# Performance work log

Measured on AMD Instinct MI355X. Metric: run time of the kernel, lower is better.

The kernel has to match this reference:

```python
import jax, jax.numpy as jnp
import numpy as np
import math

B, S, E, H = 2, 2048, 64, 8
N_LAYER = 12
EPS = 1e-5


def setup_inputs() -> dict:
    key = jax.random.key(0)
    ks = jax.random.split(key, 7)
    x = jax.random.normal(ks[0], (B, S, E), dtype=jnp.float32)
    ln_w = jnp.ones((E,), dtype=jnp.float32)
    W_q = 0.02 * jax.random.normal(ks[1], (H, E, E), dtype=jnp.float32)
    W_k = 0.02 * jax.random.normal(ks[2], (H, E, E), dtype=jnp.float32)
    W_v = 0.02 * jax.random.normal(ks[3], (H, E, E), dtype=jnp.float32)
    W_o = (0.02 / math.sqrt(2 * N_LAYER)) * jax.random.normal(ks[4], (E, H * E), dtype=jnp.float32)
    gamma = 1.0 + 0.02 * jax.random.normal(ks[5], (H, 1, 1), dtype=jnp.float32)
    return {"x": x, "ln_w": ln_w, "W_q": W_q, "W_k": W_k, "W_v": W_v, "W_o": W_o, "gamma": gamma}


def reference(x, ln_w, W_q, W_k, W_v, W_o, gamma):
    # LayerNorm (bias=False)
    mu = jnp.mean(x, axis=-1, keepdims=True)
    var = jnp.mean((x - mu) ** 2, axis=-1, keepdims=True)
    xn = (x - mu) * jax.lax.rsqrt(var + EPS) * ln_w  # [B,S,E]

    # per-head full-rank projections: x repeated across heads
    Q = jnp.einsum('bse,hef->bhsf', xn, W_q)  # [B,H,S,E]
    K = jnp.einsum('bse,hef->bhsf', xn, W_k)
    V = jnp.einsum('bse,hef->bhsf', xn, W_v)

    # RBF attention scores: exp(-gamma * ||q_i - k_j||^2 / sqrt(E)), causal
    q2 = jnp.sum(Q * Q, axis=-1)[..., :, None]          # [B,H,S,1]
    k2 = jnp.sum(K * K, axis=-1)[..., None, :]          # [B,H,1,S]
    qk = jnp.einsum('bhse,bhte->bhst', Q, K)            # [B,H,S,S]
    sqdist = q2 + k2 - 2.0 * qk
    scores = jnp.exp(-gamma[None] * sqdist / math.sqrt(E))  # gamma broadcast [H,1,1]
    causal = jnp.tril(jnp.ones((S, S), dtype=scores.dtype))
    scores = scores * causal

    out = jnp.einsum('bhst,bhte->bhse', scores, V)       # [B,H,S,E]
    out = out.transpose(0, 2, 1, 3).reshape(B, S, H * E)  # concat heads
    out = out @ W_o.T                                     # [B,S,E]
    return out
```

## Files before the change

kernel.cpp:

```cpp
#include <hip/hip_runtime.h>
#include <math.h>

typedef __attribute__((ext_vector_type(8))) short bf8;
typedef __attribute__((ext_vector_type(4))) short s4v;
typedef __attribute__((ext_vector_type(16))) float f16v;
typedef __attribute__((ext_vector_type(4))) float f4v;
typedef __attribute__((ext_vector_type(4))) int i4v;

constexpr int CS = 2048;
constexpr float EPS = 1e-5f;
constexpr float LOG2E = 1.44269504088896f;

static __device__ inline short f2bf(float x) {
  union { float f; unsigned u; } v; v.f = x;
  unsigned r = (v.u + 0x7FFFu + ((v.u >> 16) & 1u)) >> 16;
  return (short)r;
}
static __device__ inline float bf2f(short u) {
  union { unsigned u; float f; } v;
  v.u = ((unsigned)(unsigned short)u) << 16;
  return v.f;
}
static __device__ inline unsigned cvt_pk_bf16(float lo, float hi) {
  unsigned d;
  asm("v_cvt_pk_bf16_f32 %0, %1, %2" : "=v"(d) : "v"(lo), "v"(hi));
  return d;
}

__global__ __launch_bounds__(256) void k_prep(const float* __restrict__ Wq, const float* __restrict__ Wk,
                                              const float* __restrict__ Wv, const float* __restrict__ Wo,
                                              short* __restrict__ WtQ, short* __restrict__ WtK,
                                              short* __restrict__ WtV, short* __restrict__ Wob) {
  int blk = blockIdx.x, t = threadIdx.x;
  if (blk < 24) {
    __shared__ float tile[64][65];
    int w = blk >> 3, h = blk & 7;
    const float* src = (w == 0 ? Wq : w == 1 ? Wk : Wv) + h * 4096;
    short* dst = (w == 0 ? WtQ : w == 1 ? WtK : WtV) + h * 4096;
#pragma unroll
    for (int m = 0; m < 4; ++m) {
      int fi = m * 256 + t;
      int row = fi >> 4, c4 = (fi & 15) * 4;
      f4v v = *(const f4v*)&src[row * 64 + c4];
      tile[row][c4] = v.x; tile[row][c4 + 1] = v.y; tile[row][c4 + 2] = v.z; tile[row][c4 + 3] = v.w;
    }
    __syncthreads();
#pragma unroll
    for (int m = 0; m < 16; ++m) {
      int o = m * 256 + t;
      int f = o >> 6, e = o & 63;
      dst[f * 64 + e] = f2bf(tile[e][f]);
    }
  } else {
    int base = (blk - 24) * 4096;
#pragma unroll
    for (int m = 0; m < 16; ++m) {
      int o = base + m * 256 + t;
      Wob[o] = f2bf(Wo[o]);
    }
  }
}

__global__ __launch_bounds__(256) void k_qkv(const float* __restrict__ x, const float* __restrict__ ln_w,
                                             const short* __restrict__ WtQ, const short* __restrict__ WtK,
                                             const short* __restrict__ WtV, const float* __restrict__ gamma,
                                             short* __restrict__ Qf, short* __restrict__ Kf,
                                             short* __restrict__ Vf, float* __restrict__ aqg) {
  __shared__ short QtL[2 * 32 * 72];
  __shared__ short KtL[2 * 32 * 72];
  __shared__ float q2s[64];
  __shared__ float bks[64];
  int blk = blockIdx.x;
  int bh = blk & 15, st = blk >> 4;
  int b = bh >> 3, h = bh & 7;
  int t = threadIdx.x, wid = t >> 6, lane = t & 63;
  int l31 = lane & 31, g = lane >> 5;
  int sh = wid >> 1, fh = wid & 1;
  int f = fh * 32 + l31;

  int row = b * CS + st * 64 + sh * 32 + l31;
  f4v xv[8];
#pragma unroll
  for (int ks = 0; ks < 4; ++ks) {
    xv[2 * ks]     = *(const f4v*)&x[row * 64 + ks * 16 + g * 8];
    xv[2 * ks + 1] = *(const f4v*)&x[row * 64 + ks * 16 + g * 8 + 4];
  }
  float s = 0.f;
#pragma unroll
  for (int m = 0; m < 8; ++m) s += xv[m].x + xv[m].y + xv[m].z + xv[m].w;
  s += __shfl_xor(s, 32, 64);
  float mu = s * (1.f / 64.f);
  float vs = 0.f;
#pragma unroll
  for (int m = 0; m < 8; ++m) {
#pragma unroll
    for (int j = 0; j < 4; ++j) { float d = xv[m][j] - mu; vs += d * d; }
  }
  vs += __shfl_xor(vs, 32, 64);
  float rs = rsqrtf(vs * (1.f / 64.f) + EPS);
  bf8 af[4];
#pragma unroll
  for (int ks = 0; ks < 4; ++ks) {
    f4v lw0 = *(const f4v*)&ln_w[ks * 16 + g * 8];
    f4v lw1 = *(const f4v*)&ln_w[ks * 16 + g * 8 + 4];
#pragma unroll
    for (int j = 0; j < 4; ++j) {
      af[ks][j]     = f2bf((xv[2 * ks][j] - mu) * rs * lw0[j]);
      af[ks][j + 4] = f2bf((xv[2 * ks + 1][j] - mu) * rs * lw1[j]);
    }
  }
  float gh = gamma[h];
  float cgk = -gh * 0.125f * LOG2E;

  f16v cq; for (int i = 0; i < 16; ++i) cq[i] = 0.f;
#pragma unroll
  for (int ks = 0; ks < 4; ++ks) {
    bf8 bw = *(const bf8*)&WtQ[h * 4096 + f * 64 + ks * 16 + g * 8];
    cq = __builtin_amdgcn_mfma_f32_32x32x16_bf16(af[ks], bw, cq, 0, 0, 0);
  }
#pragma unroll
  for (int r = 0; r < 16; ++r) {
    int rl = (r & 3) + 8 * (r >> 2) + 4 * g;
    QtL[(sh * 32 + rl) * 72 + f] = f2bf(cq[r]);
  }
  f16v ck; for (int i = 0; i < 16; ++i) ck[i] = 0.f;
#pragma unroll
  for (int ks = 0; ks < 4; ++ks) {
    bf8 bw = *(const bf8*)&WtK[h * 4096 + f * 64 + ks * 16 + g * 8];
    ck = __builtin_amdgcn_mfma_f32_32x32x16_bf16(af[ks], bw, ck, 0, 0, 0);
  }
#pragma unroll
  for (int r = 0; r < 16; ++r) {
    int rl = (r & 3) + 8 * (r >> 2) + 4 * g;
    KtL[(sh * 32 + rl) * 72 + f] = f2bf(ck[r]);
  }
  f16v cv; for (int i = 0; i < 16; ++i) cv[i] = 0.f;
#pragma unroll
  for (int ks = 0; ks < 4; ++ks) {
    bf8 bw = *(const bf8*)&WtV[h * 4096 + f * 64 + ks * 16 + g * 8];
    cv = __builtin_amdgcn_mfma_f32_32x32x16_bf16(af[ks], bw, cv, 0, 0, 0);
  }
  __syncthreads();

  {
    int rw = t >> 2, q4 = t & 3;
    float sq = 0.f, sk = 0.f;
#pragma unroll
    for (int m = 0; m < 2; ++m) {
      bf8 vq = *(bf8*)&QtL[rw * 72 + q4 * 16 + m * 8];
      bf8 vk = *(bf8*)&KtL[rw * 72 + q4 * 16 + m * 8];
#pragma unroll
      for (int j = 0; j < 8; ++j) {
        float xq = bf2f(vq[j]); sq += xq * xq;
        float xk = bf2f(vk[j]); sk += xk * xk;
      }
    }
    sq += __shfl_xor(sq, 1, 64); sq += __shfl_xor(sq, 2, 64);
    sk += __shfl_xor(sk, 1, 64); sk += __shfl_xor(sk, 2, 64);
    if (q4 == 0) {
      q2s[rw] = sq;
      bks[rw] = exp2f(cgk * sk);
    }
  }
  {
    int ktloc = t >> 7, lm = (t >> 1) & 63, jh = t & 1;
#pragma unroll
    for (int ks = 0; ks < 4; ++ks) {
      int laddr = (ktloc * 32 + (lm & 31)) * 72 + ks * 16 + (lm >> 5) * 8 + jh * 4;
      int gaddr = ((bh * 64 + st * 2 + ktloc) * 4 + ks) * 512 + lm * 8 + jh * 4;
      *(s4v*)&Qf[gaddr] = *(s4v*)&QtL[laddr];
      *(s4v*)&Kf[gaddr] = *(s4v*)&KtL[laddr];
    }
  }
  __syncthreads();

  int kt = st * 2 + sh;
#pragma unroll
  for (int m = 0; m < 4; ++m) {
    s4v pk;
#pragma unroll
    for (int c = 0; c < 4; ++c) {
      int rl = sh * 32 + c + 8 * m + 4 * g;
      pk[c] = f2bf(cv[m * 4 + c] * bks[rl]);
    }
    int addr = ((((bh * 64 + kt) * 2 + fh) * 2 + (m >> 1)) * 64 + (m & 1) * 32 + l31) * 8 + 4 * g;
    *(s4v*)&Vf[addr] = pk;
  }
  if (t < 64) {
    aqg[bh * CS + st * 64 + t] = exp2f(cgk * q2s[t]);
  }
}

__global__ __launch_bounds__(512, 4) void k_attn(const short* __restrict__ Qf, const short* __restrict__ Kf,
                                                 const short* __restrict__ Vf, const float* __restrict__ aqg,
                                                 const float* __restrict__ gamma, short* __restrict__ attnB) {
  __shared__ float red4[4][64][37];
  int bid = blockIdx.x;
  int bh = ((bid & 7) << 1) | ((bid >> 3) & 1);
  int qt = 63 - (bid >> 4);
  int b = bh >> 3, h = bh & 7;
  int t = threadIdx.x, w = t >> 6, lane = t & 63;
  int lam = lane & 31, g = lane >> 5;
  float cg = gamma[h] * 0.25f * LOG2E;
  int L = qt + 1;
  int lo = (w * L) >> 3, hi = ((w + 1) * L) >> 3;

  bf8 qf[4];
#pragma unroll
  for (int ks = 0; ks < 4; ++ks) qf[ks] = *(const bf8*)&Qf[((bh * 64 + qt) * 4 + ks) * 512 + lane * 8];

  f16v oa0, oa1;
#pragma unroll
  for (int rr = 0; rr < 16; ++rr) { oa0[rr] = 0.f; oa1[rr] = 0.f; }

  const short* kfb = Kf + bh * 131072 + lane * 8;
  const short* vfb = Vf + bh * 131072 + lane * 8;

  for (int kt = lo; kt < hi; ++kt) {
    const short* kp = kfb + kt * 2048;
    bf8 ak0 = *(const bf8*)(kp);
    bf8 ak1 = *(const bf8*)(kp + 512);
    bf8 ak2 = *(const bf8*)(kp + 1024);
    bf8 ak3 = *(const bf8*)(kp + 1536);

    f16v ct;
#pragma unroll
    for (int rr = 0; rr < 16; ++rr) ct[rr] = 0.f;
    __builtin_amdgcn_s_setprio(1);
    ct = __builtin_amdgcn_mfma_f32_32x32x16_bf16(ak0, qf[0], ct, 0, 0, 0);
    ct = __builtin_amdgcn_mfma_f32_32x32x16_bf16(ak1, qf[1], ct, 0, 0, 0);
    ct = __builtin_amdgcn_mfma_f32_32x32x16_bf16(ak2, qf[2], ct, 0, 0, 0);
    ct = __builtin_amdgcn_mfma_f32_32x32x16_bf16(ak3, qf[3], ct, 0, 0, 0);
    __builtin_amdgcn_s_setprio(0);

    const short* vp = vfb + kt * 2048;
    bf8 av00 = *(const bf8*)(vp);
    bf8 av01 = *(const bf8*)(vp + 512);
    bf8 av10 = *(const bf8*)(vp + 1024);
    bf8 av11 = *(const bf8*)(vp + 1536);

    bool diag = (kt == qt);
    unsigned pkA[4], pkB[4];
#pragma unroll
    for (int m = 0; m < 4; ++m) {
      float sv[4];
#pragma unroll
      for (int ii = 0; ii < 4; ++ii) {
        int kloc = ii + 8 * m + 4 * g;
        float ev = exp2f(cg * ct[4 * m + ii]);
        if (diag && kloc > lam) ev = 0.f;
        sv[ii] = ev;
      }
      pkA[m] = cvt_pk_bf16(sv[0], sv[1]);
      pkB[m] = cvt_pk_bf16(sv[2], sv[3]);
    }
    __builtin_amdgcn_s_setprio(1);
#pragma unroll
    for (int ks2 = 0; ks2 < 2; ++ks2) {
      unsigned sendA = g ? pkA[2 * ks2] : pkA[2 * ks2 + 1];
      unsigned recvA = (unsigned)__shfl_xor((int)sendA, 32, 64);
      unsigned sendB = g ? pkB[2 * ks2] : pkB[2 * ks2 + 1];
      unsigned recvB = (unsigned)__shfl_xor((int)sendB, 32, 64);
      i4v wv;
      wv.x = g ? (int)recvA : (int)pkA[2 * ks2];
      wv.y = g ? (int)recvB : (int)pkB[2 * ks2];
      wv.z = g ? (int)pkA[2 * ks2 + 1] : (int)recvA;
      wv.w = g ? (int)pkB[2 * ks2 + 1] : (int)recvB;
      bf8 bs = *(bf8*)&wv;
      oa0 = __builtin_amdgcn_mfma_f32_32x32x16_bf16(ks2 ? av01 : av00, bs, oa0, 0, 0, 0);
      oa1 = __builtin_amdgcn_mfma_f32_32x32x16_bf16(ks2 ? av11 : av10, bs, oa1, 0, 0, 0);
    }
    __builtin_amdgcn_s_setprio(0);
  }

  if (w < 4) {
#pragma unroll
    for (int rr = 0; rr < 16; ++rr) {
      int e = (rr & 3) + 8 * (rr >> 2) + 4 * g;
      red4[w][e][lam] = oa0[rr];
      red4[w][e + 32][lam] = oa1[rr];
    }
  }
  __syncthreads();
  if (w >= 4) {
#pragma unroll
    for (int rr = 0; rr < 16; ++rr) {
      int e = (rr & 3) + 8 * (rr >> 2) + 4 * g;
      red4[w - 4][e][lam] += oa0[rr];
      red4[w - 4][e + 32][lam] += oa1[rr];
    }
  }
  __syncthreads();
  {
    int q = t >> 4, e0 = (t & 15) * 4;
    float aqv = aqg[bh * CS + qt * 32 + q];
    s4v ov;
#pragma unroll
    for (int jj = 0; jj < 4; ++jj) {
      float v = red4[0][e0 + jj][q] + red4[1][e0 + jj][q] + red4[2][e0 + jj][q] + red4[3][e0 + jj][q];
      ov[jj] = f2bf(v * aqv);
    }
    *(s4v*)&attnB[(b * CS + qt * 32 + q) * 512 + h * 64 + e0] = ov;
  }
}

__global__ __launch_bounds__(256) void k_proj(const short* __restrict__ attnB, const short* __restrict__ Wob,
                                              float* __restrict__ out) {
  __shared__ float red[4][32][36];
  int blk = blockIdx.x, t = threadIdx.x;
  int rt = blk >> 1, fh2 = blk & 1;
  int r0 = rt * 32;
  int kw = t >> 6, lane = t & 63, l31 = lane & 31, g = lane >> 5;
  f16v c; for (int i = 0; i < 16; ++i) c[i] = 0.f;
  int arow = (r0 + l31) * 512;
  int brow = (fh2 * 32 + l31) * 512;
#pragma unroll
  for (int ks = 0; ks < 8; ++ks) {
    int k0 = kw * 128 + ks * 16 + g * 8;
    bf8 a = *(const bf8*)&attnB[arow + k0];
    bf8 bw = *(const bf8*)&Wob[brow + k0];
    c = __builtin_amdgcn_mfma_f32_32x32x16_bf16(a, bw, c, 0, 0, 0);
  }
#pragma unroll
  for (int rr = 0; rr < 16; ++rr) {
    int rw = (rr & 3) + 8 * (rr >> 2) + 4 * g;
    red[kw][rw][l31] = c[rr];
  }
  __syncthreads();
  {
    int rw = t >> 3, f4 = (t & 7) * 4;
    f4v sum;
#pragma unroll
    for (int j = 0; j < 4; ++j)
      sum[j] = red[0][rw][f4 + j] + red[1][rw][f4 + j] + red[2][rw][f4 + j] + red[3][rw][f4 + j];
    *(f4v*)&out[(r0 + rw) * 64 + fh2 * 32 + f4] = sum;
  }
}

extern "C" void kernel_launch(void* const* d_in, const int* in_sizes, int n_in,
                              void* d_out, int out_size, void* d_ws, size_t ws_size,
                              hipStream_t stream) {
  const float* x     = (const float*)d_in[0];
  const float* ln_w  = (const float*)d_in[1];
  const float* Wq    = (const float*)d_in[2];
  const float* Wk    = (const float*)d_in[3];
  const float* Wv    = (const float*)d_in[4];
  const float* Wo    = (const float*)d_in[5];
  const float* gamma = (const float*)d_in[6];
  float* out = (float*)d_out;

  char* w = (char*)d_ws;
  short* Qf    = (short*)w;
  short* Kf    = (short*)(w + 4194304);
  short* Vf    = (short*)(w + 2 * 4194304);
  float* aqg   = (float*)(w + 3 * 4194304);
  short* attnB = (short*)(w + 3 * 4194304 + 131072);
  short* WtQ   = (short*)(w + 4 * 4194304 + 131072);
  short* WtK   = WtQ + 32768;
  short* WtV   = WtK + 32768;
  short* Wob   = WtV + 32768;

  hipLaunchKernelGGL(k_prep, dim3(32),   dim3(256), 0, stream, Wq, Wk, Wv, Wo, WtQ, WtK, WtV, Wob);
  hipLaunchKernelGGL(k_qkv,  dim3(512),  dim3(256), 0, stream, x, ln_w, WtQ, WtK, WtV, gamma, Qf, Kf, Vf, aqg);
  hipLaunchKernelGGL(k_attn, dim3(1024), dim3(512), 0, stream, Qf, Kf, Vf, aqg, gamma, attnB);
  hipLaunchKernelGGL(k_proj, dim3(256),  dim3(256), 0, stream, attnB, Wob, out);
}
```

Before: 46.49 us.

## Fuse weight prep into consumers and process two query tiles per attention block

Removes the separate weight-prep kernel. k_qkv now transposes and converts the per-head Q/K/V weights into shared memory itself, and k_proj converts Wo to bf16 on the fly. Each attention block now handles two adjacent query tiles, so every K/V tile load feeds both, halving the grid. This cuts one launch and the K/V reload traffic, but raises register pressure from four accumulators and adds redundant weight conversion in every qkv block.

After: 61.30 us. +31.8%, slower.

```diff
diff --git a/kernel.cpp b/kernel.cpp
--- a/kernel.cpp
+++ b/kernel.cpp
@@ -27,45 +27,12 @@
   return d;
 }
 
-__global__ __launch_bounds__(256) void k_prep(const float* __restrict__ Wq, const float* __restrict__ Wk,
-                                              const float* __restrict__ Wv, const float* __restrict__ Wo,
-                                              short* __restrict__ WtQ, short* __restrict__ WtK,
-                                              short* __restrict__ WtV, short* __restrict__ Wob) {
-  int blk = blockIdx.x, t = threadIdx.x;
-  if (blk < 24) {
-    __shared__ float tile[64][65];
-    int w = blk >> 3, h = blk & 7;
-    const float* src = (w == 0 ? Wq : w == 1 ? Wk : Wv) + h * 4096;
-    short* dst = (w == 0 ? WtQ : w == 1 ? WtK : WtV) + h * 4096;
-#pragma unroll
-    for (int m = 0; m < 4; ++m) {
-      int fi = m * 256 + t;
-      int row = fi >> 4, c4 = (fi & 15) * 4;
-      f4v v = *(const f4v*)&src[row * 64 + c4];
-      tile[row][c4] = v.x; tile[row][c4 + 1] = v.y; tile[row][c4 + 2] = v.z; tile[row][c4 + 3] = v.w;
-    }
-    __syncthreads();
-#pragma unroll
-    for (int m = 0; m < 16; ++m) {
-      int o = m * 256 + t;
-      int f = o >> 6, e = o & 63;
-      dst[f * 64 + e] = f2bf(tile[e][f]);
-    }
-  } else {
-    int base = (blk - 24) * 4096;
-#pragma unroll
-    for (int m = 0; m < 16; ++m) {
-      int o = base + m * 256 + t;
-      Wob[o] = f2bf(Wo[o]);
-    }
-  }
-}
-
 __global__ __launch_bounds__(256) void k_qkv(const float* __restrict__ x, const float* __restrict__ ln_w,
-                                             const short* __restrict__ WtQ, const short* __restrict__ WtK,
-                                             const short* __restrict__ WtV, const float* __restrict__ gamma,
+                                             const float* __restrict__ Wq, const float* __restrict__ Wk,
+                                             const float* __restrict__ Wv, const float* __restrict__ gamma,
                                              short* __restrict__ Qf, short* __restrict__ Kf,
                                              short* __restrict__ Vf, float* __restrict__ aqg) {
+  __shared__ short WtL[3 * 64 * 72];
   __shared__ short QtL[2 * 32 * 72];
   __shared__ short KtL[2 * 32 * 72];
   __shared__ float q2s[64];
@@ -78,6 +45,30 @@
   int sh = wid >> 1, fh = wid & 1;
   int f = fh * 32 + l31;
 
+  {
+    int e0 = (t >> 4) * 4, f0 = (t & 15) * 4;
+    const float* srcs[3];
+    srcs[0] = Wq + h * 4096; srcs[1] = Wk + h * 4096; srcs[2] = Wv + h * 4096;
+#pragma unroll
+    for (int wsel = 0; wsel < 3; ++wsel) {
+      const float* src = srcs[wsel];
+      f4v r0 = *(const f4v*)&src[(e0 + 0) * 64 + f0];
+      f4v r1 = *(const f4v*)&src[(e0 + 1) * 64 + f0];
+      f4v r2 = *(const f4v*)&src[(e0 + 2) * 64 + f0];
+      f4v r3 = *(const f4v*)&src[(e0 + 3) * 64 + f0];
+      short* dst = &WtL[wsel * 4608];
+      s4v c0, c1, c2, c3;
+      c0[0] = f2bf(r0.x); c0[1] = f2bf(r1.x); c0[2] = f2bf(r2.x); c0[3] = f2bf(r3.x);
+      c1[0] = f2bf(r0.y); c1[1] = f2bf(r1.y); c1[2] = f2bf(r2.y); c1[3] = f2bf(r3.y);
+      c2[0] = f2bf(r0.z); c2[1] = f2bf(r1.z); c2[2] = f2bf(r2.z); c2[3] = f2bf(r3.z);
+      c3[0] = f2bf(r0.w); c3[1] = f2bf(r1.w); c3[2] = f2bf(r2.w); c3[3] = f2bf(r3.w);
+      *(s4v*)&dst[(f0 + 0) * 72 + e0] = c0;
+      *(s4v*)&dst[(f0 + 1) * 72 + e0] = c1;
+      *(s4v*)&dst[(f0 + 2) * 72 + e0] = c2;
+      *(s4v*)&dst[(f0 + 3) * 72 + e0] = c3;
+    }
+  }
+
   int row = b * CS + st * 64 + sh * 32 + l31;
   f4v xv[8];
 #pragma unroll
@@ -111,11 +102,12 @@
   }
   float gh = gamma[h];
   float cgk = -gh * 0.125f * LOG2E;
+  __syncthreads();
 
   f16v cq; for (int i = 0; i < 16; ++i) cq[i] = 0.f;
 #pragma unroll
   for (int ks = 0; ks < 4; ++ks) {
-    bf8 bw = *(const bf8*)&WtQ[h * 4096 + f * 64 + ks * 16 + g * 8];
+    bf8 bw = *(const bf8*)&WtL[0 * 4608 + f * 72 + ks * 16 + g * 8];
     cq = __builtin_amdgcn_mfma_f32_32x32x16_bf16(af[ks], bw, cq, 0, 0, 0);
   }
 #pragma unroll
@@ -126,7 +118,7 @@
   f16v ck; for (int i = 0; i < 16; ++i) ck[i] = 0.f;
 #pragma unroll
   for (int ks = 0; ks < 4; ++ks) {
-    bf8 bw = *(const bf8*)&WtK[h * 4096 + f * 64 + ks * 16 + g * 8];
+    bf8 bw = *(const bf8*)&WtL[1 * 4608 + f * 72 + ks * 16 + g * 8];
     ck = __builtin_amdgcn_mfma_f32_32x32x16_bf16(af[ks], bw, ck, 0, 0, 0);
   }
 #pragma unroll
@@ -137,7 +129,7 @@
   f16v cv; for (int i = 0; i < 16; ++i) cv[i] = 0.f;
 #pragma unroll
   for (int ks = 0; ks < 4; ++ks) {
-    bf8 bw = *(const bf8*)&WtV[h * 4096 + f * 64 + ks * 16 + g * 8];
+    bf8 bw = *(const bf8*)&WtL[2 * 4608 + f * 72 + ks * 16 + g * 8];
     cv = __builtin_amdgcn_mfma_f32_32x32x16_bf16(af[ks], bw, cv, 0, 0, 0);
   }
   __syncthreads();
@@ -197,21 +189,26 @@
   __shared__ float red4[4][64][37];
   int bid = blockIdx.x;
   int bh = ((bid & 7) << 1) | ((bid >> 3) & 1);
-  int qt = 63 - (bid >> 4);
+  int z = bid >> 4;
+  int u = (z < 16) ? (31 - z) : (z - 16);
+  int qtA = 2 * u, qtB = 2 * u + 1;
   int b = bh >> 3, h = bh & 7;
   int t = threadIdx.x, w = t >> 6, lane = t & 63;
   int lam = lane & 31, g = lane >> 5;
   float cg = gamma[h] * 0.25f * LOG2E;
-  int L = qt + 1;
+  int L = qtB + 1;
   int lo = (w * L) >> 3, hi = ((w + 1) * L) >> 3;
 
-  bf8 qf[4];
-#pragma unroll
-  for (int ks = 0; ks < 4; ++ks) qf[ks] = *(const bf8*)&Qf[((bh * 64 + qt) * 4 + ks) * 512 + lane * 8];
-
-  f16v oa0, oa1;
-#pragma unroll
-  for (int rr = 0; rr < 16; ++rr) { oa0[rr] = 0.f; oa1[rr] = 0.f; }
+  bf8 qfA[4], qfB[4];
+#pragma unroll
+  for (int ks = 0; ks < 4; ++ks) {
+    qfA[ks] = *(const bf8*)&Qf[((bh * 64 + qtA) * 4 + ks) * 512 + lane * 8];
+    qfB[ks] = *(const bf8*)&Qf[((bh * 64 + qtB) * 4 + ks) * 512 + lane * 8];
+  }
+
+  f16v oaA0, oaA1, oaB0, oaB1;
+#pragma unroll
+  for (int rr = 0; rr < 16; ++rr) { oaA0[rr] = 0.f; oaA1[rr] = 0.f; oaB0[rr] = 0.f; oaB1[rr] = 0.f; }
 
   const short* kfb = Kf + bh * 131072 + lane * 8;
   const short* vfb = Vf + bh * 131072 + lane * 8;
@@ -222,15 +219,22 @@
     bf8 ak1 = *(const bf8*)(kp + 512);
     bf8 ak2 = *(const bf8*)(kp + 1024);
     bf8 ak3 = *(const bf8*)(kp + 1536);
-
-    f16v ct;
-#pragma unroll
-    for (int rr = 0; rr < 16; ++rr) ct[rr] = 0.f;
+    bool doA = (kt <= qtA);
+
+    f16v ctA, ctB;
+#pragma unroll
+    for (int rr = 0; rr < 16; ++rr) { ctA[rr] = 0.f; ctB[rr] = 0.f; }
     __builtin_amdgcn_s_setprio(1);
-    ct = __builtin_amdgcn_mfma_f32_32x32x16_bf16(ak0, qf[0], ct, 0, 0, 0);
-    ct = __builtin_amdgcn_mfma_f32_32x32x16_bf16(ak1, qf[1], ct, 0, 0, 0);
-    ct = __builtin_amdgcn_mfma_f32_32x32x16_bf16(ak2, qf[2], ct, 0, 0, 0);
-    ct = __builtin_amdgcn_mfma_f32_32x32x16_bf16(ak3, qf[3], ct, 0, 0, 0);
+    if (doA) {
+      ctA = __builtin_amdgcn_mfma_f32_32x32x16_bf16(ak0, qfA[0], ctA, 0, 0, 0);
+      ctA = __builtin_amdgcn_mfma_f32_32x32x16_bf16(ak1, qfA[1], ctA, 0, 0, 0);
+      ctA = __builtin_amdgcn_mfma_f32_32x32x16_bf16(ak2, qfA[2], ctA, 0, 0, 0);
+      ctA = __builtin_amdgcn_mfma_f32_32x32x16_bf16(ak3, qfA[3], ctA, 0, 0, 0);
+    }
+    ctB = __builtin_amdgcn_mfma_f32_32x32x16_bf16(ak0, qfB[0], ctB, 0, 0, 0);
+    ctB = __builtin_amdgcn_mfma_f32_32x32x16_bf16(ak1, qfB[1], ctB, 0, 0, 0);
+    ctB = __builtin_amdgcn_mfma_f32_32x32x16_bf16(ak2, qfB[2], ctB, 0, 0, 0);
+    ctB = __builtin_amdgcn_mfma_f32_32x32x16_bf16(ak3, qfB[3], ctB, 0, 0, 0);
     __builtin_amdgcn_s_setprio(0);
 
     const short* vp = vfb + kt * 2048;
@@ -239,36 +243,71 @@
     bf8 av10 = *(const bf8*)(vp + 1024);
     bf8 av11 = *(const bf8*)(vp + 1536);
 
-    bool diag = (kt == qt);
-    unsigned pkA[4], pkB[4];
-#pragma unroll
-    for (int m = 0; m < 4; ++m) {
-      float sv[4];
-#pragma unroll
-      for (int ii = 0; ii < 4; ++ii) {
-        int kloc = ii + 8 * m + 4 * g;
-        float ev = exp2f(cg * ct[4 * m + ii]);
-        if (diag && kloc > lam) ev = 0.f;
-        sv[ii] = ev;
+    unsigned pA0[4], pA1[4], pB0[4], pB1[4];
+    if (doA) {
+      bool dgA = (kt == qtA);
+#pragma unroll
+      for (int m = 0; m < 4; ++m) {
+        float sv[4];
+#pragma unroll
+        for (int ii = 0; ii < 4; ++ii) {
+          int kloc = ii + 8 * m + 4 * g;
+          float ev = exp2f(cg * ctA[4 * m + ii]);
+          if (dgA && kloc > lam) ev = 0.f;
+          sv[ii] = ev;
+        }
+        pA0[m] = cvt_pk_bf16(sv[0], sv[1]);
+        pA1[m] = cvt_pk_bf16(sv[2], sv[3]);
       }
-      pkA[m] = cvt_pk_bf16(sv[0], sv[1]);
-      pkB[m] = cvt_pk_bf16(sv[2], sv[3]);
+    }
+    {
+      bool dgB = (kt == qtB);
+#pragma unroll
+      for (int m = 0; m < 4; ++m) {
+        float sv[4];
+#pragma unroll
+        for (int ii = 0; ii < 4; ++ii) {
+          int kloc = ii + 8 * m + 4 * g;
+          float ev = exp2f(cg * ctB[4 * m + ii]);
+          if (dgB && kloc > lam) ev = 0.f;
+          sv[ii] = ev;
+        }
+        pB0[m] = cvt_pk_bf16(sv[0], sv[1]);
+        pB1[m] = cvt_pk_bf16(sv[2], sv[3]);
+      }
     }
     __builtin_amdgcn_s_setprio(1);
+    if (doA) {
+#pragma unroll
+      for (int ks2 = 0; ks2 < 2; ++ks2) {
+        unsigned sendA = g ? pA0[2 * ks2] : pA0[2 * ks2 + 1];
+        unsigned recvA = (unsigned)__shfl_xor((int)sendA, 32, 64);
+        unsigned sendB = g ? pA1[2 * ks2] : pA1[2 * ks2 + 1];
+        unsigned recvB = (unsigned)__shfl_xor((int)sendB, 32, 64);
+        i4v wv;
+        wv.x = g ? (int)recvA : (int)pA0[2 * ks2];
+        wv.y = g ? (int)recvB : (int)pA1[2 * ks2];
+        wv.z = g ? (int)pA0[2 * ks2 + 1] : (int)recvA;
+        wv.w = g ? (int)pA1[2 * ks2 + 1] : (int)recvB;
+        bf8 bs = *(bf8*)&wv;
+        oaA0 = __builtin_amdgcn_mfma_f32_32x32x16_bf16(ks2 ? av01 : av00, bs, oaA0, 0, 0, 0);
+        oaA1 = __builtin_amdgcn_mfma_f32_32x32x16_bf16(ks2 ? av11 : av10, bs, oaA1, 0, 0, 0);
+      }
+    }
 #pragma unroll
     for (int ks2 = 0; ks2 < 2; ++ks2) {
-      unsigned sendA = g ? pkA[2 * ks2] : pkA[2 * ks2 + 1];
+      unsigned sendA = g ? pB0[2 * ks2] : pB0[2 * ks2 + 1];
       unsigned recvA = (unsigned)__shfl_xor((int)sendA, 32, 64);
-      unsigned sendB = g ? pkB[2 * ks2] : pkB[2 * ks2 + 1];
+      unsigned sendB = g ? pB1[2 * ks2] : pB1[2 * ks2 + 1];
       unsigned recvB = (unsigned)__shfl_xor((int)sendB, 32, 64);
       i4v wv;
-      wv.x = g ? (int)recvA : (int)pkA[2 * ks2];
-      wv.y = g ? (int)recvB : (int)pkB[2 * ks2];
-      wv.z = g ? (int)pkA[2 * ks2 + 1] : (int)recvA;
-      wv.w = g ? (int)pkB[2 * ks2 + 1] : (int)recvB;
+      wv.x = g ? (int)recvA : (int)pB0[2 * ks2];
+      wv.y = g ? (int)recvB : (int)pB1[2 * ks2];
+      wv.z = g ? (int)pB0[2 * ks2 + 1] : (int)recvA;
+      wv.w = g ? (int)pB1[2 * ks2 + 1] : (int)recvB;
       bf8 bs = *(bf8*)&wv;
-      oa0 = __builtin_amdgcn_mfma_f32_32x32x16_bf16(ks2 ? av01 : av00, bs, oa0, 0, 0, 0);
-      oa1 = __builtin_amdgcn_mfma_f32_32x32x16_bf16(ks2 ? av11 : av10, bs, oa1, 0, 0, 0);
+      oaB0 = __builtin_amdgcn_mfma_f32_32x32x16_bf16(ks2 ? av01 : av00, bs, oaB0, 0, 0, 0);
+      oaB1 = __builtin_amdgcn_mfma_f32_32x32x16_bf16(ks2 ? av11 : av10, bs, oaB1, 0, 0, 0);
     }
     __builtin_amdgcn_s_setprio(0);
   }
@@ -277,8 +316,8 @@
 #pragma unroll
     for (int rr = 0; rr < 16; ++rr) {
       int e = (rr & 3) + 8 * (rr >> 2) + 4 * g;
-      red4[w][e][lam] = oa0[rr];
-      red4[w][e + 32][lam] = oa1[rr];
+      red4[w][e][lam] = oaA0[rr];
+      red4[w][e + 32][lam] = oaA1[rr];
     }
   }
   __syncthreads();
@@ -286,25 +325,55 @@
 #pragma unroll
     for (int rr = 0; rr < 16; ++rr) {
       int e = (rr & 3) + 8 * (rr >> 2) + 4 * g;
-      red4[w - 4][e][lam] += oa0[rr];
-      red4[w - 4][e + 32][lam] += oa1[rr];
+      red4[w - 4][e][lam] += oaA0[rr];
+      red4[w - 4][e + 32][lam] += oaA1[rr];
     }
   }
   __syncthreads();
   {
     int q = t >> 4, e0 = (t & 15) * 4;
-    float aqv = aqg[bh * CS + qt * 32 + q];
+    float aqv = aqg[bh * CS + qtA * 32 + q];
     s4v ov;
 #pragma unroll
     for (int jj = 0; jj < 4; ++jj) {
       float v = red4[0][e0 + jj][q] + red4[1][e0 + jj][q] + red4[2][e0 + jj][q] + red4[3][e0 + jj][q];
       ov[jj] = f2bf(v * aqv);
     }
-    *(s4v*)&attnB[(b * CS + qt * 32 + q) * 512 + h * 64 + e0] = ov;
-  }
-}
-
-__global__ __launch_bounds__(256) void k_proj(const short* __restrict__ attnB, const short* __restrict__ Wob,
+    *(s4v*)&attnB[(b * CS + qtA * 32 + q) * 512 + h * 64 + e0] = ov;
+  }
+  __syncthreads();
+  if (w < 4) {
+#pragma unroll
+    for (int rr = 0; rr < 16; ++rr) {
+      int e = (rr & 3) + 8 * (rr >> 2) + 4 * g;
+      red4[w][e][lam] = oaB0[rr];
+      red4[w][e + 32][lam] = oaB1[rr];
+    }
+  }
+  __syncthreads();
+  if (w >= 4) {
+#pragma unroll
+    for (int rr = 0; rr < 16; ++rr) {
+      int e = (rr & 3) + 8 * (rr >> 2) + 4 * g;
+      red4[w - 4][e][lam] += oaB0[rr];
+      red4[w - 4][e + 32][lam] += oaB1[rr];
+    }
+  }
+  __syncthreads();
+  {
+    int q = t >> 4, e0 = (t & 15) * 4;
+    float aqv = aqg[bh * CS + qtB * 32 + q];
+    s4v ov;
+#pragma unroll
+    for (int jj = 0; jj < 4; ++jj) {
+      float v = red4[0][e0 + jj][q] + red4[1][e0 + jj][q] + red4[2][e0 + jj][q] + red4[3][e0 + jj][q];
+      ov[jj] = f2bf(v * aqv);
+    }
+    *(s4v*)&attnB[(b * CS + qtB * 32 + q) * 512 + h * 64 + e0] = ov;
+  }
+}
+
+__global__ __launch_bounds__(256) void k_proj(const short* __restrict__ attnB, const float* __restrict__ Wo,
                                               float* __restrict__ out) {
   __shared__ float red[4][32][36];
   int blk = blockIdx.x, t = threadIdx.x;
@@ -313,12 +382,19 @@
   int kw = t >> 6, lane = t & 63, l31 = lane & 31, g = lane >> 5;
   f16v c; for (int i = 0; i < 16; ++i) c[i] = 0.f;
   int arow = (r0 + l31) * 512;
-  int brow = (fh2 * 32 + l31) * 512;
+  int fw = fh2 * 32 + l31;
 #pragma unroll
   for (int ks = 0; ks < 8; ++ks) {
     int k0 = kw * 128 + ks * 16 + g * 8;
     bf8 a = *(const bf8*)&attnB[arow + k0];
-    bf8 bw = *(const bf8*)&Wob[brow + k0];
+    f4v w0 = *(const f4v*)&Wo[fw * 512 + k0];
+    f4v w1 = *(const f4v*)&Wo[fw * 512 + k0 + 4];
+    i4v wp;
+    wp.x = (int)cvt_pk_bf16(w0.x, w0.y);
+    wp.y = (int)cvt_pk_bf16(w0.z, w0.w);
+    wp.z = (int)cvt_pk_bf16(w1.x, w1.y);
+    wp.w = (int)cvt_pk_bf16(w1.z, w1.w);
+    bf8 bw = *(bf8*)&wp;
     c = __builtin_amdgcn_mfma_f32_32x32x16_bf16(a, bw, c, 0, 0, 0);
   }
 #pragma unroll
@@ -355,13 +431,8 @@
   short* Vf    = (short*)(w + 2 * 4194304);
   float* aqg   = (float*)(w + 3 * 4194304);
   short* attnB = (short*)(w + 3 * 4194304 + 131072);
-  short* WtQ   = (short*)(w + 4 * 4194304 + 131072);
-  short* WtK   = WtQ + 32768;
-  short* WtV   = WtK + 32768;
-  short* Wob   = WtV + 32768;
-
-  hipLaunchKernelGGL(k_prep, dim3(32),   dim3(256), 0, stream, Wq, Wk, Wv, Wo, WtQ, WtK, WtV, Wob);
-  hipLaunchKernelGGL(k_qkv,  dim3(512),  dim3(256), 0, stream, x, ln_w, WtQ, WtK, WtV, gamma, Qf, Kf, Vf, aqg);
-  hipLaunchKernelGGL(k_attn, dim3(1024), dim3(512), 0, stream, Qf, Kf, Vf, aqg, gamma, attnB);
-  hipLaunchKernelGGL(k_proj, dim3(256),  dim3(256), 0, stream, attnB, Wob, out);
-}
+
+  hipLaunchKernelGGL(k_qkv,  dim3(512), dim3(256), 0, stream, x, ln_w, Wq, Wk, Wv, gamma, Qf, Kf, Vf, aqg);
+  hipLaunchKernelGGL(k_attn, dim3(512), dim3(512), 0, stream, Qf, Kf, Vf, aqg, gamma, attnB);
+  hipLaunchKernelGGL(k_proj, dim3(256), dim3(256), 0, stream, attnB, Wo, out);
+}
```

## Fuse weight prep into QKV and projection kernels; peel diagonal attention tile

Applied to the files above, without the earlier changes.

Removes the separate weight-prep kernel launch. The QKV kernel now transposes and converts W_q/W_k/W_v to bf16 in shared memory per block, and the projection kernel converts W_o from fp32 on the fly. The attention loop also peels the diagonal key tile out so the main loop carries no causal-mask check. This saves a launch and a global round trip, at the cost of repeating the weight conversion in every block and adding a shared-memory sync.

After: 41.93 us. 1.11x faster.

```diff
diff --git a/kernel.cpp b/kernel.cpp
--- a/kernel.cpp
+++ b/kernel.cpp
@@ -27,45 +27,12 @@
   return d;
 }
 
-__global__ __launch_bounds__(256) void k_prep(const float* __restrict__ Wq, const float* __restrict__ Wk,
-                                              const float* __restrict__ Wv, const float* __restrict__ Wo,
-                                              short* __restrict__ WtQ, short* __restrict__ WtK,
-                                              short* __restrict__ WtV, short* __restrict__ Wob) {
-  int blk = blockIdx.x, t = threadIdx.x;
-  if (blk < 24) {
-    __shared__ float tile[64][65];
-    int w = blk >> 3, h = blk & 7;
-    const float* src = (w == 0 ? Wq : w == 1 ? Wk : Wv) + h * 4096;
-    short* dst = (w == 0 ? WtQ : w == 1 ? WtK : WtV) + h * 4096;
-#pragma unroll
-    for (int m = 0; m < 4; ++m) {
-      int fi = m * 256 + t;
-      int row = fi >> 4, c4 = (fi & 15) * 4;
-      f4v v = *(const f4v*)&src[row * 64 + c4];
-      tile[row][c4] = v.x; tile[row][c4 + 1] = v.y; tile[row][c4 + 2] = v.z; tile[row][c4 + 3] = v.w;
-    }
-    __syncthreads();
-#pragma unroll
-    for (int m = 0; m < 16; ++m) {
-      int o = m * 256 + t;
-      int f = o >> 6, e = o & 63;
-      dst[f * 64 + e] = f2bf(tile[e][f]);
-    }
-  } else {
-    int base = (blk - 24) * 4096;
-#pragma unroll
-    for (int m = 0; m < 16; ++m) {
-      int o = base + m * 256 + t;
-      Wob[o] = f2bf(Wo[o]);
-    }
-  }
-}
-
 __global__ __launch_bounds__(256) void k_qkv(const float* __restrict__ x, const float* __restrict__ ln_w,
-                                             const short* __restrict__ WtQ, const short* __restrict__ WtK,
-                                             const short* __restrict__ WtV, const float* __restrict__ gamma,
+                                             const float* __restrict__ Wq, const float* __restrict__ Wk,
+                                             const float* __restrict__ Wv, const float* __restrict__ gamma,
                                              short* __restrict__ Qf, short* __restrict__ Kf,
                                              short* __restrict__ Vf, float* __restrict__ aqg) {
+  __shared__ short WtL[3 * 64 * 72];
   __shared__ short QtL[2 * 32 * 72];
   __shared__ short KtL[2 * 32 * 72];
   __shared__ float q2s[64];
@@ -78,6 +45,30 @@
   int sh = wid >> 1, fh = wid & 1;
   int f = fh * 32 + l31;
 
+  {
+    int e0 = (t >> 4) * 4, f0 = (t & 15) * 4;
+    const float* srcs[3];
+    srcs[0] = Wq + h * 4096; srcs[1] = Wk + h * 4096; srcs[2] = Wv + h * 4096;
+#pragma unroll
+    for (int wsel = 0; wsel < 3; ++wsel) {
+      const float* src = srcs[wsel];
+      f4v r0 = *(const f4v*)&src[(e0 + 0) * 64 + f0];
+      f4v r1 = *(const f4v*)&src[(e0 + 1) * 64 + f0];
+      f4v r2 = *(const f4v*)&src[(e0 + 2) * 64 + f0];
+      f4v r3 = *(const f4v*)&src[(e0 + 3) * 64 + f0];
+      short* dst = &WtL[wsel * 4608];
+      s4v c0, c1, c2, c3;
+      c0[0] = f2bf(r0.x); c0[1] = f2bf(r1.x); c0[2] = f2bf(r2.x); c0[3] = f2bf(r3.x);
+      c1[0] = f2bf(r0.y); c1[1] = f2bf(r1.y); c1[2] = f2bf(r2.y); c1[3] = f2bf(r3.y);
+      c2[0] = f2bf(r0.z); c2[1] = f2bf(r1.z); c2[2] = f2bf(r2.z); c2[3] = f2bf(r3.z);
+      c3[0] = f2bf(r0.w); c3[1] = f2bf(r1.w); c3[2] = f2bf(r2.w); c3[3] = f2bf(r3.w);
+      *(s4v*)&dst[(f0 + 0) * 72 + e0] = c0;
+      *(s4v*)&dst[(f0 + 1) * 72 + e0] = c1;
+      *(s4v*)&dst[(f0 + 2) * 72 + e0] = c2;
+      *(s4v*)&dst[(f0 + 3) * 72 + e0] = c3;
+    }
+  }
+
   int row = b * CS + st * 64 + sh * 32 + l31;
   f4v xv[8];
 #pragma unroll
@@ -111,11 +102,12 @@
   }
   float gh = gamma[h];
   float cgk = -gh * 0.125f * LOG2E;
+  __syncthreads();
 
   f16v cq; for (int i = 0; i < 16; ++i) cq[i] = 0.f;
 #pragma unroll
   for (int ks = 0; ks < 4; ++ks) {
-    bf8 bw = *(const bf8*)&WtQ[h * 4096 + f * 64 + ks * 16 + g * 8];
+    bf8 bw = *(const bf8*)&WtL[0 * 4608 + f * 72 + ks * 16 + g * 8];
     cq = __builtin_amdgcn_mfma_f32_32x32x16_bf16(af[ks], bw, cq, 0, 0, 0);
   }
 #pragma unroll
@@ -126,7 +118,7 @@
   f16v ck; for (int i = 0; i < 16; ++i) ck[i] = 0.f;
 #pragma unroll
   for (int ks = 0; ks < 4; ++ks) {
-    bf8 bw = *(const bf8*)&WtK[h * 4096 + f * 64 + ks * 16 + g * 8];
+    bf8 bw = *(const bf8*)&WtL[1 * 4608 + f * 72 + ks * 16 + g * 8];
     ck = __builtin_amdgcn_mfma_f32_32x32x16_bf16(af[ks], bw, ck, 0, 0, 0);
   }
 #pragma unroll
@@ -137,7 +129,7 @@
   f16v cv; for (int i = 0; i < 16; ++i) cv[i] = 0.f;
 #pragma unroll
   for (int ks = 0; ks < 4; ++ks) {
-    bf8 bw = *(const bf8*)&WtV[h * 4096 + f * 64 + ks * 16 + g * 8];
+    bf8 bw = *(const bf8*)&WtL[2 * 4608 + f * 72 + ks * 16 + g * 8];
     cv = __builtin_amdgcn_mfma_f32_32x32x16_bf16(af[ks], bw, cv, 0, 0, 0);
   }
   __syncthreads();
@@ -204,6 +196,7 @@
   float cg = gamma[h] * 0.25f * LOG2E;
   int L = qt + 1;
   int lo = (w * L) >> 3, hi = ((w + 1) * L) >> 3;
+  int hiND = hi < qt ? hi : qt;
 
   bf8 qf[4];
 #pragma unroll
@@ -216,7 +209,7 @@
   const short* kfb = Kf + bh * 131072 + lane * 8;
   const short* vfb = Vf + bh * 131072 + lane * 8;
 
-  for (int kt = lo; kt < hi; ++kt) {
+  for (int kt = lo; kt < hiND; ++kt) {
     const short* kp = kfb + kt * 2048;
     bf8 ak0 = *(const bf8*)(kp);
     bf8 ak1 = *(const bf8*)(kp + 512);
@@ -239,20 +232,15 @@
     bf8 av10 = *(const bf8*)(vp + 1024);
     bf8 av11 = *(const bf8*)(vp + 1536);
 
-    bool diag = (kt == qt);
     unsigned pkA[4], pkB[4];
 #pragma unroll
     for (int m = 0; m < 4; ++m) {
-      float sv[4];
-#pragma unroll
-      for (int ii = 0; ii < 4; ++ii) {
-        int kloc = ii + 8 * m + 4 * g;
-        float ev = exp2f(cg * ct[4 * m + ii]);
-        if (diag && kloc > lam) ev = 0.f;
-        sv[ii] = ev;
-      }
-      pkA[m] = cvt_pk_bf16(sv[0], sv[1]);
-      pkB[m] = cvt_pk_bf16(sv[2], sv[3]);
+      float e0 = exp2f(cg * ct[4 * m + 0]);
+      float e1 = exp2f(cg * ct[4 * m + 1]);
+      float e2 = exp2f(cg * ct[4 * m + 2]);
+      float e3 = exp2f(cg * ct[4 * m + 3]);
+      pkA[m] = cvt_pk_bf16(e0, e1);
+      pkB[m] = cvt_pk_bf16(e2, e3);
     }
     __builtin_amdgcn_s_setprio(1);
 #pragma unroll
@@ -273,6 +261,59 @@
     __builtin_amdgcn_s_setprio(0);
   }
 
+  if (hi > hiND) {
+    int kt = qt;
+    const short* kp = kfb + kt * 2048;
+    bf8 ak0 = *(const bf8*)(kp);
+    bf8 ak1 = *(const bf8*)(kp + 512);
+    bf8 ak2 = *(const bf8*)(kp + 1024);
+    bf8 ak3 = *(const bf8*)(kp + 1536);
+
+    f16v ct;
+#pragma unroll
+    for (int rr = 0; rr < 16; ++rr) ct[rr] = 0.f;
+    ct = __builtin_amdgcn_mfma_f32_32x32x16_bf16(ak0, qf[0], ct, 0, 0, 0);
+    ct = __builtin_amdgcn_mfma_f32_32x32x16_bf16(ak1, qf[1], ct, 0, 0, 0);
+    ct = __builtin_amdgcn_mfma_f32_32x32x16_bf16(ak2, qf[2], ct, 0, 0, 0);
+    ct = __builtin_amdgcn_mfma_f32_32x32x16_bf16(ak3, qf[3], ct, 0, 0, 0);
+
+    const short* vp = vfb + kt * 2048;
+    bf8 av00 = *(const bf8*)(vp);
+    bf8 av01 = *(const bf8*)(vp + 512);
+    bf8 av10 = *(const bf8*)(vp + 1024);
+    bf8 av11 = *(const bf8*)(vp + 1536);
+
+    unsigned pkA[4], pkB[4];
+#pragma unroll
+    for (int m = 0; m < 4; ++m) {
+      float sv[4];
+#pragma unroll
+      for (int ii = 0; ii < 4; ++ii) {
+        int kloc = ii + 8 * m + 4 * g;
+        float ev = exp2f(cg * ct[4 * m + ii]);
+        if (kloc > lam) ev = 0.f;
+        sv[ii] = ev;
+      }
+      pkA[m] = cvt_pk_bf16(sv[0], sv[1]);
+      pkB[m] = cvt_pk_bf16(sv[2], sv[3]);
+    }
+#pragma unroll
+    for (int ks2 = 0; ks2 < 2; ++ks2) {
+      unsigned sendA = g ? pkA[2 * ks2] : pkA[2 * ks2 + 1];
+      unsigned recvA = (unsigned)__shfl_xor((int)sendA, 32, 64);
+      unsigned sendB = g ? pkB[2 * ks2] : pkB[2 * ks2 + 1];
+      unsigned recvB = (unsigned)__shfl_xor((int)sendB, 32, 64);
+      i4v wv;
+      wv.x = g ? (int)recvA : (int)pkA[2 * ks2];
+      wv.y = g ? (int)recvB : (int)pkB[2 * ks2];
+      wv.z = g ? (int)pkA[2 * ks2 + 1] : (int)recvA;
+      wv.w = g ? (int)pkB[2 * ks2 + 1] : (int)recvB;
+      bf8 bs = *(bf8*)&wv;
+      oa0 = __builtin_amdgcn_mfma_f32_32x32x16_bf16(ks2 ? av01 : av00, bs, oa0, 0, 0, 0);
+      oa1 = __builtin_amdgcn_mfma_f32_32x32x16_bf16(ks2 ? av11 : av10, bs, oa1, 0, 0, 0);
+    }
+  }
+
   if (w < 4) {
 #pragma unroll
     for (int rr = 0; rr < 16; ++rr) {
@@ -304,7 +345,7 @@
   }
 }
 
-__global__ __launch_bounds__(256) void k_proj(const short* __restrict__ attnB, const short* __restrict__ Wob,
+__global__ __launch_bounds__(256) void k_proj(const short* __restrict__ attnB, const float* __restrict__ Wo,
                                               float* __restrict__ out) {
   __shared__ float red[4][32][36];
   int blk = blockIdx.x, t = threadIdx.x;
@@ -313,12 +354,19 @@
   int kw = t >> 6, lane = t & 63, l31 = lane & 31, g = lane >> 5;
   f16v c; for (int i = 0; i < 16; ++i) c[i] = 0.f;
   int arow = (r0 + l31) * 512;
-  int brow = (fh2 * 32 + l31) * 512;
+  int fw = fh2 * 32 + l31;
 #pragma unroll
   for (int ks = 0; ks < 8; ++ks) {
     int k0 = kw * 128 + ks * 16 + g * 8;
     bf8 a = *(const bf8*)&attnB[arow + k0];
-    bf8 bw = *(const bf8*)&Wob[brow + k0];
+    f4v w0 = *(const f4v*)&Wo[fw * 512 + k0];
+    f4v w1 = *(const f4v*)&Wo[fw * 512 + k0 + 4];
+    i4v wp;
+    wp.x = (int)cvt_pk_bf16(w0.x, w0.y);
+    wp.y = (int)cvt_pk_bf16(w0.z, w0.w);
+    wp.z = (int)cvt_pk_bf16(w1.x, w1.y);
+    wp.w = (int)cvt_pk_bf16(w1.z, w1.w);
+    bf8 bw = *(bf8*)&wp;
     c = __builtin_amdgcn_mfma_f32_32x32x16_bf16(a, bw, c, 0, 0, 0);
   }
 #pragma unroll
@@ -355,13 +403,8 @@
   short* Vf    = (short*)(w + 2 * 4194304);
   float* aqg   = (float*)(w + 3 * 4194304);
   short* attnB = (short*)(w + 3 * 4194304 + 131072);
-  short* WtQ   = (short*)(w + 4 * 4194304 + 131072);
-  short* WtK   = WtQ + 32768;
-  short* WtV   = WtK + 32768;
-  short* Wob   = WtV + 32768;
-
-  hipLaunchKernelGGL(k_prep, dim3(32),   dim3(256), 0, stream, Wq, Wk, Wv, Wo, WtQ, WtK, WtV, Wob);
-  hipLaunchKernelGGL(k_qkv,  dim3(512),  dim3(256), 0, stream, x, ln_w, WtQ, WtK, WtV, gamma, Qf, Kf, Vf, aqg);
+
+  hipLaunchKernelGGL(k_qkv,  dim3(512),  dim3(256), 0, stream, x, ln_w, Wq, Wk, Wv, gamma, Qf, Kf, Vf, aqg);
   hipLaunchKernelGGL(k_attn, dim3(1024), dim3(512), 0, stream, Qf, Kf, Vf, aqg, gamma, attnB);
-  hipLaunchKernelGGL(k_proj, dim3(256),  dim3(256), 0, stream, attnB, Wob, out);
-}
+  hipLaunchKernelGGL(k_proj, dim3(256),  dim3(256), 0, stream, attnB, Wo, out);
+}
```
